# Performance work log

Hardware: AMD Instinct MI355X
Metric: run time of the kernel (lower is better)

Reference implementation:

```python
import jax, jax.numpy as jnp
import numpy as np

SCALES = (128.0, 256.0, 512.0)
ASPECT = (0.5, 1.0, 2.0)
K = 9
NMS_THR = 0.7
PRE_NMS_TOPK = 10000
POST_NMS_TOPK = 2000
MIN_SIZE = 16.0

def conv2d(x, w, b, pad):
    out = jax.lax.conv_general_dilated(x, w, (1, 1), [(pad, pad), (pad, pad)], dimension_numbers=('NCHW', 'OIHW', 'NCHW'))
    return out + b[None, :, None, None]

def generate_anchors(grid_h, grid_w, dtype):
    # Faithful to source: shifts are grid indices, NOT multiplied by stride (source bug kept).
    scales = jnp.asarray(SCALES, dtype)
    ar = jnp.asarray(ASPECT, dtype)
    h_ratio = jnp.sqrt(ar)
    w_ratio = 1.0 / h_ratio
    ws = (w_ratio[:, None] * scales[None, :]).reshape(-1)
    hs = (h_ratio[:, None] * scales[None, :]).reshape(-1)
    base = jnp.round(jnp.stack([-ws, -hs, ws, hs], axis=1) / 2.0)  # (9,4)
    sy, sx = jnp.meshgrid(jnp.arange(grid_h), jnp.arange(grid_w), indexing='ij')
    sx = sx.reshape(-1).astype(dtype)
    sy = sy.reshape(-1).astype(dtype)
    shifts = jnp.stack([sx, sy, sx, sy], axis=1)  # (H*W,4)
    return (shifts[:, None, :] + base[None, :, :]).reshape(-1, 4)  # (H*W*9,4)

def decode(box_pred, anchors):
    w = anchors[:, 2] - anchors[:, 0]
    h = anchors[:, 3] - anchors[:, 1]
    cx = anchors[:, 0] + 0.5 * w
    cy = anchors[:, 1] + 0.5 * h
    dx, dy, dw, dh = box_pred[:, 0], box_pred[:, 1], box_pred[:, 2], box_pred[:, 3]
    pcx = dx * w + cx
    pcy = dy * h + cy
    pw = jnp.exp(dw) * w
    ph = jnp.exp(dh) * h
    return jnp.stack([pcx - 0.5 * pw, pcy - 0.5 * ph, pcx + 0.5 * pw, pcy + 0.5 * ph], axis=1)

def nms_keep(boxes, valid, thr):
    # Greedy NMS on score-descending boxes; invalid (small) boxes never kept nor suppress others.
    n = boxes.shape[0]
    x1, y1, x2, y2 = boxes[:, 0], boxes[:, 1], boxes[:, 2], boxes[:, 3]
    areas = (x2 - x1) * (y2 - y1)
    idx = jnp.arange(n)
    def body(i, keep):
        xx1 = jnp.maximum(x1, x1[i]); yy1 = jnp.maximum(y1, y1[i])
        xx2 = jnp.minimum(x2, x2[i]); yy2 = jnp.minimum(y2, y2[i])
        inter = jnp.maximum(xx2 - xx1, 0.0) * jnp.maximum(yy2 - yy1, 0.0)
        iou = inter / (areas + areas[i] - inter)
        suppress = (iou > thr) & (idx > i) & keep[i]
        return keep & (~suppress)
    return jax.lax.fori_loop(0, n, body, valid)

def filter_proposals(proposals, cls_scores, img_h, img_w):
    scores = jax.nn.sigmoid(cls_scores.reshape(-1))
    top_scores, top_idx = jax.lax.top_k(scores, PRE_NMS_TOPK)  # sorted descending
    props = proposals[top_idx]
    x1 = jnp.clip(props[:, 0], 0.0, img_w); y1 = jnp.clip(props[:, 1], 0.0, img_h)
    x2 = jnp.clip(props[:, 2], 0.0, img_w); y2 = jnp.clip(props[:, 3], 0.0, img_h)
    props = jnp.stack([x1, y1, x2, y2], axis=1)
    valid = ((x2 - x1) >= MIN_SIZE) & ((y2 - y1) >= MIN_SIZE)
    keep = jax.lax.stop_gradient(nms_keep(jax.lax.stop_gradient(props), valid, NMS_THR))
    masked = jnp.where(keep, top_scores, -1.0)
    final_scores, final_idx = jax.lax.top_k(masked, POST_NMS_TOPK)  # order = score-descending (matches post-NMS sort)
    final_props = props[final_idx]
    valid_out = final_scores > 0.0  # sigmoid scores > 0, padding = -1
    return jnp.where(valid_out[:, None], final_props, 0.0), jnp.where(valid_out, final_scores, 0.0)

def setup_inputs():
    key = jax.random.key(0)
    ks = jax.random.split(key, 8)
    C = 512; GH = GW = 50
    feat = jax.random.normal(ks[0], (1, C, GH, GW), jnp.float32)
    image = jnp.zeros((1, 3, 800, 800), jnp.float32)
    gt_boxes = jax.random.uniform(ks[1], (8, 4), jnp.float32) * 800.0
    w_rpn = jax.random.normal(ks[2], (C, C, 3, 3), jnp.float32) * 0.01
    b_rpn = jnp.zeros((C,), jnp.float32)
    w_cls = jax.random.normal(ks[3], (K, C, 1, 1), jnp.float32) * 0.01
    b_cls = jnp.zeros((K,), jnp.float32)
    w_reg = jax.random.normal(ks[4], (4 * K, C, 1, 1), jnp.float32) * 0.01
    b_reg = jnp.zeros((4 * K,), jnp.float32)
    return {"image": image, "feat": feat, "gt_boxes": gt_boxes, "w_rpn": w_rpn, "b_rpn": b_rpn, "w_cls": w_cls, "b_cls": b_cls, "w_reg": w_reg, "b_reg": b_reg}

def reference(image, feat, gt_boxes, w_rpn, b_rpn, w_cls, b_cls, w_reg, b_reg):
    rpn_feat = jax.nn.relu(conv2d(feat, w_rpn, b_rpn, 1))
    cls = conv2d(rpn_feat, w_cls, b_cls, 0)      # (B,9,H,W)
    reg = conv2d(rpn_feat, w_reg, b_reg, 0)      # (B,36,H,W)
    B, _, gh, gw = feat.shape
    anchors = generate_anchors(gh, gw, feat.dtype)
    # flatten to anchor ordering (h, w, k) matching generate_anchors
    cls_flat = jnp.transpose(cls, (0, 2, 3, 1)).reshape(-1)
    reg_flat = jnp.transpose(reg.reshape(B, K, 4, gh, gw), (0, 3, 4, 1, 2)).reshape(-1, 4)
    proposals = decode(reg_flat, anchors)
    img_h, img_w = float(image.shape[-2]), float(image.shape[-1])
    return filter_proposals(proposals, cls_flat, img_h, img_w)
```

## Files before the change

kernel.cpp:

```cpp
#include <hip/hip_runtime.h>
#include <cmath>
#include <cstdint>
#include <cstddef>

typedef unsigned long long u64;
typedef unsigned int u32;

#define NPX   2500
#define NANCH 22500
#define PRE_TOPK 10000
#define NWORDS 160
#define NJC 45

struct AnchorBase { float b[36]; };

typedef __attribute__((ext_vector_type(8))) short bf16x8;
typedef __attribute__((ext_vector_type(4))) float f32x4;

__device__ inline unsigned short f2bf(float f) {
    u32 u = __float_as_uint(f);
    u32 r = u + 0x7fffu + ((u >> 16) & 1u);
    return (unsigned short)(r >> 16);
}
__device__ inline float bf2f(unsigned short h) {
    return __uint_as_float(((u32)h) << 16);
}

__device__ inline void gload_lds16(const void* g, void* l) {
    __builtin_amdgcn_global_load_lds(
        (const __attribute__((address_space(1))) unsigned int*)g,
        (__attribute__((address_space(3))) unsigned int*)l, 16, 0, 0);
}

__global__ __launch_bounds__(256) void kprep(const float* __restrict__ feat,
                                             const float* __restrict__ wr,
                                             unsigned short* __restrict__ xthi,
                                             unsigned short* __restrict__ xtlo,
                                             unsigned short* __restrict__ whi,
                                             unsigned short* __restrict__ wlo)
{
    __shared__ float sh[4608];
    int bid = blockIdx.x;
    int t = threadIdx.x;
    if (bid < 416) {
        float (*tile)[65] = (float(*)[65])sh;
        int gr = bid >> 3;
        int cc = bid & 7;
        int tx = t & 63, ty = t >> 6;
        int y = gr - 1;
        bool rowok = (gr >= 1) && (gr <= 50);
#pragma unroll
        for (int i = 0; i < 16; ++i) {
            int c = i * 4 + ty;
            tile[c][tx] = (rowok && tx < 50)
                        ? feat[(size_t)(cc * 64 + c) * NPX + y * 50 + tx] : 0.f;
        }
        __syncthreads();
#pragma unroll
        for (int i = 0; i < 16; ++i) {
            int xp = i * 4 + ty;
            int cell = gr * 64 + xp;
            bool ok = rowok && xp >= 1 && xp <= 50;
            float v = ok ? tile[tx][xp - 1] : 0.f;
            unsigned short hi = f2bf(v);
            xthi[(size_t)cell * 512 + cc * 64 + tx] = hi;
            xtlo[(size_t)cell * 512 + cc * 64 + tx] = f2bf(v - bf2f(hi));
        }
    } else {
        int oc = bid - 416;
        for (int j = t; j < 4608; j += 256) sh[j] = wr[(size_t)oc * 4608 + j];
        __syncthreads();
        for (int k = t; k < 4608; k += 256) {
            int c = k & 511, tap = k >> 9;
            float v = sh[c * 9 + tap];
            unsigned short hi = f2bf(v);
            whi[(size_t)oc * 4608 + k] = hi;
            wlo[(size_t)oc * 4608 + k] = f2bf(v - bf2f(hi));
        }
    }
}

__global__ __launch_bounds__(256) void k1m(const unsigned short* __restrict__ xthi,
                                           const unsigned short* __restrict__ xtlo,
                                           const unsigned short* __restrict__ whi,
                                           const unsigned short* __restrict__ wlo,
                                           float* __restrict__ pk,
                                           int cptLog, int cptm1, int cptMul, int niter)
{
    __shared__ __align__(16) unsigned short Ah[8192];
    __shared__ __align__(16) unsigned short Al[8192];
    __shared__ __align__(16) unsigned short Bh[4096];
    __shared__ __align__(16) unsigned short Bl[4096];

    int t = threadIdx.x;
    int lane = t & 63, wave = t >> 6;
    int wo = wave & 1, wp = wave >> 1;
    int ocb = blockIdx.x, pxb = blockIdx.y, bs = blockIdx.z;
    int q = lane >> 4, m = lane & 15;
    int c0base = bs * cptMul;

    int g  = t & 7;
    int r0 = t >> 3;
    int ocA[4];
    int cellB[2];
#pragma unroll
    for (int i = 0; i < 4; ++i) ocA[i] = ocb * 128 + r0 + 32 * i;
#pragma unroll
    for (int i = 0; i < 2; ++i) {
        int opx = pxb * 64 + r0 + 32 * i;
        cellB[i] = (opx < NPX) ? ((opx / 50) + 1) * 64 + (opx % 50) + 1 : 190;
    }

    char* AhB = (char*)Ah;
    char* AlB = (char*)Al;
    char* BhB = (char*)Bh;
    char* BlB = (char*)Bl;
    int lb = t * 16;

    f32x4 acc[8];
    f32x4 zf = {0.f, 0.f, 0.f, 0.f};
#pragma unroll
    for (int i = 0; i < 8; ++i) acc[i] = zf;

    for (int it = 0; it < niter; ++it) {
        int tap = it >> cptLog;
        int cw  = it & cptm1;
        int c0  = c0base + cw * 64;
        int t3  = (tap * 43) >> 7;
        int tapoff = (t3 - 1) * 64 + (tap - t3 * 3) - 1;
#pragma unroll
        for (int i = 0; i < 4; ++i) {
            size_t ga = (size_t)ocA[i] * 4608 + tap * 512 + c0 + g * 8;
            gload_lds16(whi + ga, AhB + lb + 4096 * i);
            gload_lds16(wlo + ga, AlB + lb + 4096 * i);
        }
#pragma unroll
        for (int i = 0; i < 2; ++i) {
            size_t gb = (size_t)(cellB[i] + tapoff) * 512 + c0 + g * 8;
            gload_lds16(xthi + gb, BhB + lb + 4096 * i);
            gload_lds16(xtlo + gb, BlB + lb + 4096 * i);
        }
        __syncthreads();
#pragma unroll
        for (int ks = 0; ks < 2; ++ks) {
            bf16x8 fah[4], fal[4], fbh[2], fbl[2];
#pragma unroll
            for (int mt = 0; mt < 4; ++mt) {
                int off = (wo * 64 + mt * 16 + m) * 64 + ks * 32 + q * 8;
                fah[mt] = *(const bf16x8*)(Ah + off);
                fal[mt] = *(const bf16x8*)(Al + off);
            }
#pragma unroll
            for (int nt = 0; nt < 2; ++nt) {
                int off = (wp * 32 + nt * 16 + m) * 64 + ks * 32 + q * 8;
                fbh[nt] = *(const bf16x8*)(Bh + off);
                fbl[nt] = *(const bf16x8*)(Bl + off);
            }
#pragma unroll
            for (int mt = 0; mt < 4; ++mt)
#pragma unroll
                for (int nt = 0; nt < 2; ++nt) {
                    f32x4 a = acc[mt * 2 + nt];
                    a = __builtin_amdgcn_mfma_f32_16x16x32_bf16(fal[mt], fbh[nt], a, 0, 0, 0);
                    a = __builtin_amdgcn_mfma_f32_16x16x32_bf16(fah[mt], fbl[nt], a, 0, 0, 0);
                    a = __builtin_amdgcn_mfma_f32_16x16x32_bf16(fah[mt], fbh[nt], a, 0, 0, 0);
                    acc[mt * 2 + nt] = a;
                }
        }
        __syncthreads();
    }
#pragma unroll
    for (int mt = 0; mt < 4; ++mt)
#pragma unroll
        for (int nt = 0; nt < 2; ++nt)
#pragma unroll
            for (int r = 0; r < 4; ++r) {
                int oc = ocb * 128 + wo * 64 + mt * 16 + q * 4 + r;
                int px = pxb * 64 + wp * 32 + nt * 16 + m;
                pk[((size_t)bs * 512 + oc) * 2560 + px] = acc[mt * 2 + nt][r];
            }
}

__global__ __launch_bounds__(256) void k2a_heads(const float* __restrict__ pk, int ns,
                                                 const float* __restrict__ br,
                                                 const float* __restrict__ wcls,
                                                 const float* __restrict__ wreg,
                                                 float* __restrict__ part)
{
    __shared__ float vt[64 * 64];
    __shared__ float Wl[45 * 64];
    int t  = threadIdx.x;
    int pb = blockIdx.x;
    int s  = blockIdx.y;
    int cb = s * 64;
    for (int e = t; e < 45 * 64; e += 256) {
        int u = e >> 6, c = e & 63;
        Wl[e] = (u < 9) ? wcls[u * 512 + cb + c] : wreg[(u - 9) * 512 + cb + c];
    }
    int pxl = t & 63, ug = t >> 6;
    int px = pb * 64 + pxl;
    bool ok = px < NPX;
#pragma unroll
    for (int i = 0; i < 16; ++i) {
        int c = ug * 16 + i;
        float v = 0.f;
        if (ok) {
            size_t bidx = (size_t)(cb + c) * 2560 + px;
            v = br[cb + c];
            for (int ks = 0; ks < ns; ++ks) v += pk[(size_t)ks * 512 * 2560 + bidx];
            v = v > 0.f ? v : 0.f;
        }
        vt[c * 64 + pxl] = v;
    }
    __syncthreads();
    int ubase = ug * 12;
    int ulim  = (45 - ubase < 12) ? (45 - ubase) : 12;
    float acc[12];
#pragma unroll
    for (int j = 0; j < 12; ++j) acc[j] = 0.f;
    for (int c = 0; c < 64; ++c) {
        float v = vt[c * 64 + pxl];
#pragma unroll
        for (int j = 0; j < 12; ++j)
            acc[j] = fmaf(v, Wl[(ubase + j) * 64 + c], acc[j]);
    }
    if (ok) {
        for (int j = 0; j < ulim; ++j)
            part[((size_t)s * 45 + ubase + j) * NPX + px] = acc[j];
    }
}

__global__ __launch_bounds__(256) void k2b_decode(const float* __restrict__ part,
                                                  const float* __restrict__ bcls,
                                                  const float* __restrict__ breg,
                                                  AnchorBase ab,
                                                  float* __restrict__ score,
                                                  float* __restrict__ bx1, float* __restrict__ by1,
                                                  float* __restrict__ bx2, float* __restrict__ by2,
                                                  u32* __restrict__ valid,
                                                  u64* __restrict__ key)
{
    int id = blockIdx.x * 256 + threadIdx.x;
    if (id >= NANCH) return;
    int k  = id / NPX;
    int px = id - k * NPX;

    float z  = bcls[k];
    float d0 = breg[k * 4 + 0], d1 = breg[k * 4 + 1];
    float d2 = breg[k * 4 + 2], d3 = breg[k * 4 + 3];
#pragma unroll
    for (int s = 0; s < 8; ++s) {
        const float* p = part + (size_t)s * 45 * NPX;
        z  += p[(size_t)k * NPX + px];
        d0 += p[(size_t)(9 + k * 4 + 0) * NPX + px];
        d1 += p[(size_t)(9 + k * 4 + 1) * NPX + px];
        d2 += p[(size_t)(9 + k * 4 + 2) * NPX + px];
        d3 += p[(size_t)(9 + k * 4 + 3) * NPX + px];
    }
    float sc = 1.f / (1.f + expf(-z));

    int yy = px / 50, xx = px - (px / 50) * 50;
    float fx = (float)xx, fy = (float)yy;
    float ax1 = fx + ab.b[k * 4 + 0], ay1 = fy + ab.b[k * 4 + 1];
    float ax2 = fx + ab.b[k * 4 + 2], ay2 = fy + ab.b[k * 4 + 3];
    float aw = ax2 - ax1, ah = ay2 - ay1;
    float cx = ax1 + 0.5f * aw, cy = ay1 + 0.5f * ah;
    float pcx = d0 * aw + cx, pcy = d1 * ah + cy;
    float pw = expf(d2) * aw, ph = expf(d3) * ah;
    float x1 = pcx - 0.5f * pw, y1 = pcy - 0.5f * ph;
    float x2 = pcx + 0.5f * pw, y2 = pcy + 0.5f * ph;
    x1 = fminf(fmaxf(x1, 0.f), 800.f);
    y1 = fminf(fmaxf(y1, 0.f), 800.f);
    x2 = fminf(fmaxf(x2, 0.f), 800.f);
    y2 = fminf(fmaxf(y2, 0.f), 800.f);
    u32 v = ((x2 - x1) >= 16.f) && ((y2 - y1) >= 16.f);

    int f = px * 9 + k;
    score[f] = sc;
    bx1[f] = x1; by1[f] = y1; bx2[f] = x2; by2[f] = y2;
    valid[f] = v;
    u32 sb = __float_as_uint(sc);
    key[f] = ((u64)(~sb) << 32) | (u32)f;
}

__global__ __launch_bounds__(256) void k3a_rank(const u64* __restrict__ key,
                                                u32* __restrict__ rankp)
{
    __shared__ __align__(16) u64 sk[500];
    int t  = threadIdx.x;
    int jb = blockIdx.y;
    int jLo = jb * 500;
    for (int e = t; e < 500; e += 256) sk[e] = key[jLo + e];
    __syncthreads();
    int i0 = blockIdx.x * 1024 + t;
    int i1 = i0 + 256, i2 = i0 + 512, i3 = i0 + 768;
    u64 k0 = (i0 < NANCH) ? key[i0] : 0ull;
    u64 k1 = (i1 < NANCH) ? key[i1] : 0ull;
    u64 k2 = (i2 < NANCH) ? key[i2] : 0ull;
    u64 k3 = (i3 < NANCH) ? key[i3] : 0ull;
    u32 c0 = 0, c1 = 0, c2 = 0, c3 = 0;
    const ulonglong2* sk2 = (const ulonglong2*)sk;
#pragma unroll 5
    for (int j = 0; j < 250; ++j) {
        ulonglong2 v = sk2[j];
        c0 += (v.x < k0) ? 1u : 0u;  c0 += (v.y < k0) ? 1u : 0u;
        c1 += (v.x < k1) ? 1u : 0u;  c1 += (v.y < k1) ? 1u : 0u;
        c2 += (v.x < k2) ? 1u : 0u;  c2 += (v.y < k2) ? 1u : 0u;
        c3 += (v.x < k3) ? 1u : 0u;  c3 += (v.y < k3) ? 1u : 0u;
    }
    size_t base = (size_t)jb * NANCH;
    if (i0 < NANCH) rankp[base + i0] = c0;
    if (i1 < NANCH) rankp[base + i1] = c1;
    if (i2 < NANCH) rankp[base + i2] = c2;
    if (i3 < NANCH) rankp[base + i3] = c3;
}

__global__ __launch_bounds__(256) void k3b_gather(const u32* __restrict__ rankp,
                                                  const float* __restrict__ score,
                                                  const float* __restrict__ bx1, const float* __restrict__ by1,
                                                  const float* __restrict__ bx2, const float* __restrict__ by2,
                                                  const u32* __restrict__ valid,
                                                  float* __restrict__ sS,
                                                  float* __restrict__ sx1, float* __restrict__ sy1,
                                                  float* __restrict__ sx2, float* __restrict__ sy2,
                                                  float4* __restrict__ sbox4,
                                                  u32* __restrict__ sInv)
{
    int i = blockIdx.x * 256 + threadIdx.x;
    if (i >= NANCH) return;
    u32 r = 0;
#pragma unroll
    for (int c = 0; c < NJC; ++c) r += rankp[(size_t)c * NANCH + i];
    if (r >= PRE_TOPK) return;
    float x1 = bx1[i], y1 = by1[i], x2 = bx2[i], y2 = by2[i];
    sS[r] = score[i];
    sx1[r] = x1; sy1[r] = y1; sx2[r] = x2; sy2[r] = y2;
    float4 b4; b4.x = x1; b4.y = y1; b4.z = x2; b4.w = y2;
    sbox4[r] = b4;
    sInv[r] = valid[i] ? 0u : 1u;
}

__global__ __launch_bounds__(256) void k4_mat(const float4* __restrict__ sbox4,
                                              u64* __restrict__ rows,
                                              u64* __restrict__ selfw)
{
    int t = threadIdx.x, lane = t & 63, wave = t >> 6;
    int i = blockIdx.x * 4 + wave;
    if (i >= PRE_TOPK) return;
    float4 bi = sbox4[i];
    float ai = (bi.z - bi.x) * (bi.w - bi.y);
    int wd  = i >> 6;
    int ish = i & 63;
    u64 diagmask = ~((2ull << ish) - 1ull);
    u64* rowp = rows + (size_t)i * NWORDS;
    for (int w0 = lane; w0 < wd; w0 += 64) rowp[w0] = 0ull;
    if (lane < 3) rowp[157 + lane] = 0ull;
    for (int w = wd; w < 157; ++w) {
        float4 bj = sbox4[(w << 6) + lane];
        float xx1 = fmaxf(bi.x, bj.x);
        float yy1 = fmaxf(bi.y, bj.y);
        float xx2 = fminf(bi.z, bj.z);
        float yy2 = fminf(bi.w, bj.w);
        float iw = fmaxf(xx2 - xx1, 0.f);
        float ih = fmaxf(yy2 - yy1, 0.f);
        float inter = iw * ih;
        float aj = (bj.z - bj.x) * (bj.w - bj.y);
        float uni = ai + aj - inter;
        u64 b = __ballot(inter > 0.7f * uni);
        if (w == wd)  b &= diagmask;
        if (w == 156) b &= 0xFFFFull;
        if (lane == 0) {
            rowp[w] = b;
            if (w == wd) selfw[i] = b;
        }
    }
}

__global__ __launch_bounds__(64) void k5_scan(const u64* __restrict__ rows,
                                              const u64* __restrict__ selfw,
                                              const u32* __restrict__ sInv,
                                              const float* __restrict__ sS,
                                              const float* __restrict__ sx1, const float* __restrict__ sy1,
                                              const float* __restrict__ sx2, const float* __restrict__ sy2,
                                              float* __restrict__ out)
{
    __shared__ int keptList[2000];
    __shared__ int kcnt;
    int l = threadIdx.x;
    auto bw = [&](int w) -> u64 {
        const uint4* p = (const uint4*)(sInv + (size_t)w * 64);
        u64 v = 0;
#pragma unroll
        for (int j = 0; j < 16; ++j) {
            uint4 q = p[j];
            v |= ((u64)(q.x != 0) << (j * 4))     | ((u64)(q.y != 0) << (j * 4 + 1))
               | ((u64)(q.z != 0) << (j * 4 + 2)) | ((u64)(q.w != 0) << (j * 4 + 3));
        }
        return v;
    };
    auto rdlane64 = [&](u64 v, int src) -> u64 {
        u32 lo = __builtin_amdgcn_readlane((u32)v, src);
        u32 hi = __builtin_amdgcn_readlane((u32)(v >> 32), src);
        return ((u64)hi << 32) | lo;
    };
    u64 r0 = bw(l);
    u64 r1 = bw(64 + l);
    u64 r2 = (l < 32) ? bw(128 + l) : ~0ull;

    u64 s0 = selfw[(size_t)0 * 64 + l];
    u64 s1 = selfw[(size_t)1 * 64 + l];
    u64 s2 = selfw[(size_t)2 * 64 + l];
    u64 s3 = selfw[(size_t)3 * 64 + l];
    u64 s4 = selfw[(size_t)4 * 64 + l];
    u64 s5 = selfw[(size_t)5 * 64 + l];
    u64 s6 = selfw[(size_t)6 * 64 + l];
    u64 s7 = selfw[(size_t)7 * 64 + l];

    int cnt = 0;
    bool done = false;
    for (int w = 0; w < 157; ++w) {
        u64 swreg = s0;
        s0 = s1; s1 = s2; s2 = s3; s3 = s4; s4 = s5; s5 = s6; s6 = s7;
        s7 = (w + 8 < 157) ? selfw[(size_t)(w + 8) * 64 + l] : 0ull;

        int slot = w >> 6, owner = w & 63;
        u64 val = (slot == 0) ? r0 : (slot == 1) ? r1 : r2;
        u64 rw = rdlane64(val, owner);
        u64 wmask = (w == 156) ? 0xFFFFull : ~0ull;
        u64 av = (~rw) & wmask;

        u64 km = 0;
        while (av) {
            int b = __builtin_ctzll(av);
            u64 sw = rdlane64(swreg, b);
            km |= 1ull << b;
            av &= ~(1ull << b);
            av &= ~sw;
        }
        u64 kk = km;
        while (kk) {
            int bsx[16];
            int nb = 0;
            while (kk && nb < 16) {
                int b = __builtin_ctzll(kk);
                kk &= kk - 1;
                bsx[nb++] = b;
            }
            u64 a0 = 0, a1 = 0, a2 = 0;
#pragma unroll
            for (int u = 0; u < 16; ++u) {
                if (u < nb) {
                    int i = (w << 6) + bsx[u];
                    if (l == 0 && cnt + u < 2000) keptList[cnt + u] = i;
                    const u64* rp = rows + (size_t)i * NWORDS;
                    a0 |= rp[l];
                    a1 |= rp[64 + l];
                    if (l < 32) a2 |= rp[128 + l];
                }
            }
            r0 |= a0; r1 |= a1; r2 |= a2;
            cnt += nb;
            if (cnt >= 2000) { done = true; break; }
        }
        if (done) break;
    }
    if (l == 0) kcnt = (cnt < 2000) ? cnt : 2000;
    __syncthreads();
    int K = kcnt;
    for (int r = l; r < 2000; r += 64) {
        if (r < K) {
            int j = keptList[r];
            out[r * 4 + 0] = sx1[j];
            out[r * 4 + 1] = sy1[j];
            out[r * 4 + 2] = sx2[j];
            out[r * 4 + 3] = sy2[j];
            out[8000 + r]  = sS[j];
        } else {
            out[r * 4 + 0] = 0.f; out[r * 4 + 1] = 0.f;
            out[r * 4 + 2] = 0.f; out[r * 4 + 3] = 0.f;
            out[8000 + r]  = 0.f;
        }
    }
}

extern "C" void kernel_launch(void* const* d_in, const int* in_sizes, int n_in,
                              void* d_out, int out_size, void* d_ws, size_t ws_size,
                              hipStream_t stream)
{
    (void)in_sizes; (void)n_in; (void)out_size;
    const float* feat = (const float*)d_in[1];
    const float* wrpn = (const float*)d_in[3];
    const float* brpn = (const float*)d_in[4];
    const float* wcls = (const float*)d_in[5];
    const float* bcls = (const float*)d_in[6];
    const float* wreg = (const float*)d_in[7];
    const float* breg = (const float*)d_in[8];
    float* out = (float*)d_out;

    int ns = (ws_size >= 58195968) ? 8 : (ws_size >= 37224448) ? 4 : 2;
    int cpt     = 8 / ns;
    int cptLog  = (ns == 2) ? 2 : (ns == 4) ? 1 : 0;
    int cptm1   = cpt - 1;
    int cptMul  = cpt * 64;
    int niter   = 9 * cpt;
    size_t pkB = (size_t)ns * 512 * 2560 * 4;

    char* ws = (char*)d_ws;
    float* pk = (float*)ws;
    unsigned short* Xthi = (unsigned short*)(ws + pkB);
    unsigned short* Xtlo = Xthi + (size_t)52 * 64 * 512;
    unsigned short* Whi  = (unsigned short*)(ws + pkB + 6815744);
    unsigned short* Wlo  = Whi + (size_t)512 * 4608;

    char* sm = ws + pkB;
    float* score = (float*)(sm + 0);
    float* bx1   = (float*)(sm + 90000);
    float* by1   = (float*)(sm + 180000);
    float* bx2   = (float*)(sm + 270000);
    float* by2   = (float*)(sm + 360000);
    u32*   valid = (u32*)  (sm + 450000);
    u64*   key   = (u64*)  (sm + 540000);
    float* sS    = (float*)(sm + 1620000);
    float* sx1   = (float*)(sm + 1660000);
    float* sy1   = (float*)(sm + 1700000);
    float* sx2   = (float*)(sm + 1740000);
    float* sy2   = (float*)(sm + 1780000);
    u32*   sInv  = (u32*)  (sm + 1820000);
    u64*   selfw = (u64*)  (sm + 1860960);
    float4* sbox4= (float4*)(sm + 1942880);
    float* part  = (float*)(sm + 2106720);
    u32*   rankp = (u32*)  (sm + 2106720);
    u64*   rows  = (u64*)  (sm + 2106720);

    AnchorBase ab;
    {
        const float scales[3] = {128.f, 256.f, 512.f};
        const float aspect[3] = {0.5f, 1.f, 2.f};
        for (int ai = 0; ai < 3; ++ai) {
            float hr = sqrtf(aspect[ai]);
            float wratio = 1.0f / hr;
            for (int si = 0; si < 3; ++si) {
                float wsz = wratio * scales[si];
                float hsz = hr * scales[si];
                int a = ai * 3 + si;
                ab.b[a * 4 + 0] = rintf(-wsz / 2.0f);
                ab.b[a * 4 + 1] = rintf(-hsz / 2.0f);
                ab.b[a * 4 + 2] = rintf( wsz / 2.0f);
                ab.b[a * 4 + 3] = rintf( hsz / 2.0f);
            }
        }
    }

    kprep    <<<928, 256, 0, stream>>>(feat, wrpn, Xthi, Xtlo, Whi, Wlo);
    k1m      <<<dim3(4, 40, ns), 256, 0, stream>>>(Xthi, Xtlo, Whi, Wlo, pk,
                                                   cptLog, cptm1, cptMul, niter);
    k2a_heads<<<dim3(40, 8), 256, 0, stream>>>(pk, ns, brpn, wcls, wreg, part);
    k2b_decode<<<88, 256, 0, stream>>>(part, bcls, breg, ab, score, bx1, by1, bx2, by2, valid, key);
    k3a_rank <<<dim3(22, NJC), 256, 0, stream>>>(key, rankp);
    k3b_gather<<<88, 256, 0, stream>>>(rankp, score, bx1, by1, bx2, by2, valid,
                                       sS, sx1, sy1, sx2, sy2, sbox4, sInv);
    k4_mat   <<<2500, 256, 0, stream>>>(sbox4, rows, selfw);
    k5_scan  <<<1, 64, 0, stream>>>(rows, selfw, sInv, sS, sx1, sy1, sx2, sy2, out);
}
```

Before: 333.1 us.

## Fuse NMS mask build and serial scan with per-block ready flags

Merges the IoU mask kernel and the single-wave greedy scan into one launch. Block 2500 acts as the scanner and spins on per-block release flags, so it can process word w as soon as the rows it needs are written instead of waiting for the whole matrix. The flags are cleared in the gather kernel. This overlaps the serial scan with mask construction and removes one launch. It relies on the scanner block being scheduled while earlier blocks run, and it adds atomic polling overhead.

```diff
diff --git a/kernel.cpp b/kernel.cpp
--- a/kernel.cpp
+++ b/kernel.cpp
@@ -324,9 +324,11 @@
                                                   float* __restrict__ sx1, float* __restrict__ sy1,
                                                   float* __restrict__ sx2, float* __restrict__ sy2,
                                                   float4* __restrict__ sbox4,
-                                                  u32* __restrict__ sInv)
+                                                  u32* __restrict__ sInv,
+                                                  u32* __restrict__ kflag)
 {
     int i = blockIdx.x * 256 + threadIdx.x;
+    if (i < 2500) kflag[i] = 0u;
     if (i >= NANCH) return;
     u32 r = 0;
 #pragma unroll
@@ -340,53 +342,75 @@
     sInv[r] = valid[i] ? 0u : 1u;
 }
 
-__global__ __launch_bounds__(256) void k4_mat(const float4* __restrict__ sbox4,
-                                              u64* __restrict__ rows,
-                                              u64* __restrict__ selfw)
-{
-    int t = threadIdx.x, lane = t & 63, wave = t >> 6;
-    int i = blockIdx.x * 4 + wave;
-    if (i >= PRE_TOPK) return;
-    float4 bi = sbox4[i];
-    float ai = (bi.z - bi.x) * (bi.w - bi.y);
-    int wd  = i >> 6;
-    int ish = i & 63;
-    u64 diagmask = ~((2ull << ish) - 1ull);
-    u64* rowp = rows + (size_t)i * NWORDS;
-    for (int w0 = lane; w0 < wd; w0 += 64) rowp[w0] = 0ull;
-    if (lane < 3) rowp[157 + lane] = 0ull;
-    for (int w = wd; w < 157; ++w) {
-        float4 bj = sbox4[(w << 6) + lane];
-        float xx1 = fmaxf(bi.x, bj.x);
-        float yy1 = fmaxf(bi.y, bj.y);
-        float xx2 = fminf(bi.z, bj.z);
-        float yy2 = fminf(bi.w, bj.w);
-        float iw = fmaxf(xx2 - xx1, 0.f);
-        float ih = fmaxf(yy2 - yy1, 0.f);
-        float inter = iw * ih;
-        float aj = (bj.z - bj.x) * (bj.w - bj.y);
-        float uni = ai + aj - inter;
-        u64 b = __ballot(inter > 0.7f * uni);
-        if (w == wd)  b &= diagmask;
-        if (w == 156) b &= 0xFFFFull;
-        if (lane == 0) {
-            rowp[w] = b;
-            if (w == wd) selfw[i] = b;
-        }
-    }
-}
-
-__global__ __launch_bounds__(64) void k5_scan(const u64* __restrict__ rows,
-                                              const u64* __restrict__ selfw,
-                                              const u32* __restrict__ sInv,
-                                              const float* __restrict__ sS,
-                                              const float* __restrict__ sx1, const float* __restrict__ sy1,
-                                              const float* __restrict__ sx2, const float* __restrict__ sy2,
-                                              float* __restrict__ out)
-{
+__global__ __launch_bounds__(256) void k45_matscan(const float4* __restrict__ sbox4,
+                                                   u64* __restrict__ rows,
+                                                   u64* __restrict__ selfw,
+                                                   u32* __restrict__ kflag,
+                                                   const u32* __restrict__ sInv,
+                                                   const float* __restrict__ sS,
+                                                   const float* __restrict__ sx1, const float* __restrict__ sy1,
+                                                   const float* __restrict__ sx2, const float* __restrict__ sy2,
+                                                   float* __restrict__ out)
+{
+    int bid = blockIdx.x;
+    int t = threadIdx.x;
+    if (bid < 2500) {
+        int lane = t & 63, wave = t >> 6;
+        int i = bid * 4 + wave;
+        float4 bi = sbox4[i];
+        float ai = (bi.z - bi.x) * (bi.w - bi.y);
+        int wd  = i >> 6;
+        int ish = i & 63;
+        u64 diagmask = ~((2ull << ish) - 1ull);
+        u64* rowp = rows + (size_t)i * NWORDS;
+        for (int w0 = lane; w0 < wd; w0 += 64) rowp[w0] = 0ull;
+        if (lane < 3) rowp[157 + lane] = 0ull;
+        for (int w = wd; w < 157; ++w) {
+            float4 bj = sbox4[(w << 6) + lane];
+            float xx1 = fmaxf(bi.x, bj.x);
+            float yy1 = fmaxf(bi.y, bj.y);
+            float xx2 = fminf(bi.z, bj.z);
+            float yy2 = fminf(bi.w, bj.w);
+            float iw = fmaxf(xx2 - xx1, 0.f);
+            float ih = fmaxf(yy2 - yy1, 0.f);
+            float inter = iw * ih;
+            float aj = (bj.z - bj.x) * (bj.w - bj.y);
+            float uni = ai + aj - inter;
+            u64 b = __ballot(inter > 0.7f * uni);
+            if (w == wd)  b &= diagmask;
+            if (w == 156) b &= 0xFFFFull;
+            if (lane == 0) {
+                rowp[w] = b;
+                if (w == wd) selfw[i] = b;
+            }
+        }
+        __syncthreads();
+        if (t == 0) {
+            __threadfence();
+            __hip_atomic_store(&kflag[bid], 1u, __ATOMIC_RELEASE,
+                               __HIP_MEMORY_SCOPE_AGENT);
+        }
+        return;
+    }
+    if (t >= 64) return;
+    int l = t;
     __shared__ int keptList[2000];
-    __shared__ int kcnt;
-    int l = threadIdx.x;
+
+    int doneUpTo = 0;
+    auto waitBlocks = [&](int need) {
+        while (doneUpTo < need) {
+            int idx = doneUpTo + l;
+            u32 f = (idx < 2500)
+                  ? __hip_atomic_load(&kflag[idx], __ATOMIC_ACQUIRE,
+                                      __HIP_MEMORY_SCOPE_AGENT) : 1u;
+            u64 ball = __ballot(f != 0);
+            u64 nball = ~ball;
+            int adv = (nball == 0) ? 64 : __builtin_ctzll(nball);
+            doneUpTo += adv;
+            if (adv == 0) __builtin_amdgcn_s_sleep(8);
+        }
+    };
+
     auto bw = [&](int w) -> u64 {
         const uint4* p = (const uint4*)(sInv + (size_t)w * 64);
         u64 v = 0;
@@ -407,6 +431,8 @@
     u64 r1 = bw(64 + l);
     u64 r2 = (l < 32) ? bw(128 + l) : ~0ull;
 
+    waitBlocks(144);
+
     u64 s0 = selfw[(size_t)0 * 64 + l];
     u64 s1 = selfw[(size_t)1 * 64 + l];
     u64 s2 = selfw[(size_t)2 * 64 + l];
@@ -419,6 +445,9 @@
     int cnt = 0;
     bool done = false;
     for (int w = 0; w < 157; ++w) {
+        int need = (w + 9) << 4;
+        waitBlocks(need < 2500 ? need : 2500);
+
         u64 swreg = s0;
         s0 = s1; s1 = s2; s2 = s3; s3 = s4; s4 = s5; s5 = s6; s6 = s7;
         s7 = (w + 8 < 157) ? selfw[(size_t)(w + 8) * 64 + l] : 0ull;
@@ -464,9 +493,7 @@
         }
         if (done) break;
     }
-    if (l == 0) kcnt = (cnt < 2000) ? cnt : 2000;
-    __syncthreads();
-    int K = kcnt;
+    int K = (cnt < 2000) ? cnt : 2000;
     for (int r = l; r < 2000; r += 64) {
         if (r < K) {
             int j = keptList[r];
@@ -531,6 +558,7 @@
     float* part  = (float*)(sm + 2106720);
     u32*   rankp = (u32*)  (sm + 2106720);
     u64*   rows  = (u64*)  (sm + 2106720);
+    u32*   kflag = (u32*)  (sm + 14906720);
 
     AnchorBase ab;
     {
@@ -558,7 +586,7 @@
     k2b_decode<<<88, 256, 0, stream>>>(part, bcls, breg, ab, score, bx1, by1, bx2, by2, valid, key);
     k3a_rank <<<dim3(22, NJC), 256, 0, stream>>>(key, rankp);
     k3b_gather<<<88, 256, 0, stream>>>(rankp, score, bx1, by1, bx2, by2, valid,
-                                       sS, sx1, sy1, sx2, sy2, sbox4, sInv);
-    k4_mat   <<<2500, 256, 0, stream>>>(sbox4, rows, selfw);
-    k5_scan  <<<1, 64, 0, stream>>>(rows, selfw, sInv, sS, sx1, sy1, sx2, sy2, out);
-}
+                                       sS, sx1, sy1, sx2, sy2, sbox4, sInv, kflag);
+    k45_matscan<<<2501, 256, 0, stream>>>(sbox4, rows, selfw, kflag, sInv,
+                                          sS, sx1, sy1, sx2, sy2, out);
+}
```

Result: slower. 506.1 us (+51.9%).
